# Kernel tuning notes

Measured on AMD Instinct MI355X. Metric: run time of the kernel, lower is better.

The kernel has to match this reference:

```python
import jax, jax.numpy as jnp
import numpy as np

NUM_HEADS = 8
LN_EPS = 1e-5


def setup_inputs() -> dict:
    key = jax.random.key(0)
    ks = jax.random.split(key, 8)
    B, H, W, C = 2, 64, 64, 256
    return {
        "x": jax.random.normal(ks[0], (B, H, W, C), dtype=jnp.float32),
        "cond": jax.random.normal(ks[1], (B, C), dtype=jnp.float32),
        "t": jax.random.randint(ks[2], (B,), 0, 100, dtype=jnp.int64),
        "emb_table": jax.random.normal(ks[3], (100, C), dtype=jnp.float32) * 0.02,
        "ada_w": jax.random.normal(ks[4], (C, 2 * C), dtype=jnp.float32) * 0.02,
        "ada_b": jnp.zeros((2 * C,), dtype=jnp.float32),
        "qkv_w": jax.random.normal(ks[5], (C, 3 * C), dtype=jnp.float32) * 0.02,
        "qkv_b": jnp.zeros((3 * C,), dtype=jnp.float32),
        "proj_w": jax.random.normal(ks[6], (C, C), dtype=jnp.float32) * 0.02,
        "proj_b": jnp.zeros((C,), dtype=jnp.float32),
    }


def reference(x, cond, t, emb_table, ada_w, ada_b, qkv_w, qkv_b, proj_w, proj_b):
    B, H, W, C = x.shape
    N = H * W
    h = NUM_HEADS
    d = C // h
    scale = d ** -0.5

    x = x.reshape(B, N, C)

    # AdaLayerNorm (adalayernorm_abs): timestep embedding -> SiLU -> Linear -> scale/shift
    emb = emb_table[t]                                # [B, C]
    ss = jax.nn.silu(emb) @ ada_w + ada_b             # [B, 2C]
    sc, sh = jnp.split(ss, 2, axis=-1)                # each [B, C]
    mu = jnp.mean(x, axis=-1, keepdims=True)
    var = jnp.var(x, axis=-1, keepdims=True)
    xn = (x - mu) * jax.lax.rsqrt(var + LN_EPS)       # LN without affine
    x = xn * (1.0 + sc[:, None, :]) + sh[:, None, :]

    # QKV projection and head split
    qkv = (x @ qkv_w + qkv_b).reshape(B, N, 3, h, d)
    qkv = jnp.transpose(qkv, (2, 0, 3, 1, 4))          # [3, B, h, N, d]
    q, k, v = qkv[0], qkv[1], qkv[2]

    # Manual attention: full [B, h, N, N] scores (matches original module)
    attn = jnp.einsum('bhnd,bhmd->bhnm', q, k) * scale
    attn = jax.nn.softmax(attn, axis=-1)
    out = jnp.einsum('bhnm,bhmd->bhnd', attn, v)       # [B, h, N, d]
    out = jnp.transpose(out, (0, 2, 1, 3)).reshape(B, N, C)

    out = (out.reshape(B, H, W, C) @ proj_w) + proj_b
    return out
```

## Files before the change

kernel.cpp:

```cpp
#include <hip/hip_runtime.h>
#include <hip/hip_bf16.h>
#include <stdint.h>

typedef __attribute__((ext_vector_type(8))) short bfrag;
typedef __attribute__((ext_vector_type(4))) short bfrag4;
typedef __attribute__((ext_vector_type(4))) float f32x4;
typedef __attribute__((ext_vector_type(2))) float f32x2;
typedef __attribute__((ext_vector_type(2))) unsigned int u32x2;

__device__ inline short f2bf(float f) {
  union { float f; uint32_t u; } v; v.f = f;
  uint32_t u = v.u;
  uint32_t r = (u + 0x7fffu + ((u >> 16) & 1u)) >> 16;
  return (short)r;
}

#if __has_builtin(__builtin_amdgcn_cvt_pk_bf16_f32)
typedef __attribute__((ext_vector_type(2))) __bf16 bf16x2_t;
__device__ inline uint32_t pack_bf16(float a, float b) {
  bf16x2_t r = __builtin_amdgcn_cvt_pk_bf16_f32(a, b);
  return __builtin_bit_cast(uint32_t, r);
}
#else
__device__ inline uint32_t pack_bf16(float a, float b) {
  uint32_t ua = __builtin_bit_cast(uint32_t, a) + 0x8000u;
  uint32_t ub = __builtin_bit_cast(uint32_t, b) + 0x8000u;
  return __builtin_amdgcn_perm(ub, ua, 0x07060302);
}
#endif

__global__ __launch_bounds__(256) void ada_kernel(
    const float* __restrict__ emb_table, const int* __restrict__ t,
    const float* __restrict__ ada_w, const float* __restrict__ ada_b,
    float* __restrict__ scsh) {
  int b = blockIdx.y;
  int tid = threadIdx.x;
  __shared__ float se[256];
  __shared__ float part[256];
  int tt = t[b];
  float e = emb_table[tt * 256 + tid];
  se[tid] = e / (1.f + __expf(-e));
  __syncthreads();
  int ol = tid & 63, kc = tid >> 6;
  int o = blockIdx.x * 64 + ol;
  float acc = 0.f;
#pragma unroll 8
  for (int k = kc * 64; k < (kc + 1) * 64; ++k) acc += se[k] * ada_w[k * 512 + o];
  part[tid] = acc;
  __syncthreads();
  if (tid < 64) {
    int oo = blockIdx.x * 64 + tid;
    scsh[b * 512 + oo] =
        part[tid] + part[64 + tid] + part[128 + tid] + part[192 + tid] + ada_b[oo];
  }
}

__global__ __launch_bounds__(256) void transpose_w(const float* __restrict__ W,
                                                   short* __restrict__ Wt, int N) {
  __shared__ float tile[64][65];
  int k0 = blockIdx.x * 64, n0 = blockIdx.y * 64;
  int tid = threadIdx.x;
  int r = tid >> 2, c0 = (tid & 3) * 16;
  const float* src = W + (long)(k0 + r) * N + n0 + c0;
#pragma unroll
  for (int j = 0; j < 16; j += 4) {
    float4 v = *(const float4*)(src + j);
    tile[r][c0 + j] = v.x; tile[r][c0 + j + 1] = v.y;
    tile[r][c0 + j + 2] = v.z; tile[r][c0 + j + 3] = v.w;
  }
  __syncthreads();
  int nl = tid >> 2, kc = (tid & 3) * 16;
  short outv[16];
#pragma unroll
  for (int j = 0; j < 16; ++j) outv[j] = f2bf(tile[kc + j][nl]);
  short* dst = Wt + (long)(n0 + nl) * 256 + k0 + kc;
  *(bfrag*)dst = *(bfrag*)&outv[0];
  *(bfrag*)(dst + 8) = *(bfrag*)&outv[8];
}

__global__ __launch_bounds__(256) void ln_kernel(const float* __restrict__ x,
                                                 const float* __restrict__ scsh,
                                                 short* __restrict__ xb) {
  int row = blockIdx.x;
  int b = row >> 12;
  int i = threadIdx.x;
  float v = x[(long)row * 256 + i];
  float s = v, sq = v * v;
#pragma unroll
  for (int off = 32; off > 0; off >>= 1) {
    s += __shfl_down(s, off);
    sq += __shfl_down(sq, off);
  }
  __shared__ float red[8];
  int w = i >> 6;
  if ((i & 63) == 0) { red[w] = s; red[4 + w] = sq; }
  __syncthreads();
  s = red[0] + red[1] + red[2] + red[3];
  sq = red[4] + red[5] + red[6] + red[7];
  float mu = s * (1.f / 256.f);
  float var = sq * (1.f / 256.f) - mu * mu;
  float xn = (v - mu) * rsqrtf(var + 1e-5f);
  float y = xn * (1.f + scsh[b * 512 + i]) + scsh[b * 512 + 256 + i];
  xb[(long)row * 256 + i] = f2bf(y);
}

__global__ __launch_bounds__(256) void gemm_bf16(const short* __restrict__ A,
                                                 const short* __restrict__ Bt,
                                                 const float* __restrict__ bias,
                                                 int N, int mode, float qscale,
                                                 short* __restrict__ qk,
                                                 short* __restrict__ vT,
                                                 float* __restrict__ cout) {
  __shared__ short As[64 * 40];
  __shared__ short Bs[64 * 40];
  const int mt = blockIdx.x, nt = blockIdx.y;
  const int tid = threadIdx.x;
  const int w = tid >> 6, lane = tid & 63, l16 = lane & 15, quad = lane >> 4;
  const int si = tid >> 2, sk = (tid & 3) * 8;
  f32x4 acc[4] = {{0,0,0,0},{0,0,0,0},{0,0,0,0},{0,0,0,0}};
  const short* Arow = A + (long)(mt * 64 + si) * 256 + sk;
  const short* Brow = Bt + (long)(nt * 64 + si) * 256 + sk;
  for (int kk = 0; kk < 8; ++kk) {
    __syncthreads();
    *(bfrag*)&As[si * 40 + sk] = *(const bfrag*)(Arow + kk * 32);
    *(bfrag*)&Bs[si * 40 + sk] = *(const bfrag*)(Brow + kk * 32);
    __syncthreads();
    bfrag a = *(const bfrag*)&As[(w * 16 + l16) * 40 + quad * 8];
#pragma unroll
    for (int c = 0; c < 4; ++c) {
      bfrag bf = *(const bfrag*)&Bs[(c * 16 + l16) * 40 + quad * 8];
      acc[c] = __builtin_amdgcn_mfma_f32_16x16x32_bf16(a, bf, acc[c], 0, 0, 0);
    }
  }
  const int row0 = mt * 64 + w * 16 + quad * 4;
  if (mode == 1) {
#pragma unroll
    for (int c = 0; c < 4; ++c) {
      int col = nt * 64 + c * 16 + l16;
      float bv = bias[col];
#pragma unroll
      for (int r = 0; r < 4; ++r)
        cout[(long)(row0 + r) * N + col] = acc[c][r] + bv;
    }
  } else if (nt < 8) {
#pragma unroll
    for (int c = 0; c < 4; ++c) {
      int col = nt * 64 + c * 16 + l16;
      float bv = bias[col];
      float mult = (col < 256) ? qscale : 1.0f;
#pragma unroll
      for (int r = 0; r < 4; ++r)
        qk[(long)(row0 + r) * 512 + col] = f2bf((acc[c][r] + bv) * mult);
    }
  } else {
    const int bb = mt >> 6;
    const int keyl = row0 & 4095;
#pragma unroll
    for (int c = 0; c < 4; ++c) {
      int col = nt * 64 + c * 16 + l16;
      float bv = bias[col];
      int d = col - 512;
      u32x2 dd;
      dd.x = pack_bf16(acc[c][0] + bv, acc[c][1] + bv);
      dd.y = pack_bf16(acc[c][2] + bv, acc[c][3] + bv);
      *(u32x2*)&vT[((long)(bb * 8 + (d >> 5)) * 32 + (d & 31)) * 4096 + keyl] = dd;
    }
  }
}

__global__ __launch_bounds__(256) void attn_kernel(const short* __restrict__ qk,
                                                   const short* __restrict__ vT,
                                                   float* __restrict__ Opart,
                                                   float* __restrict__ lpart) {
  const int blk = blockIdx.x;
  const int qt = blk & 31;
  const int bh = (blk >> 5) & 15;
  const int ks = blk >> 9;
  const int b = bh >> 3, hh = bh & 7;
  const int tid = threadIdx.x;
  const int w = tid >> 6, lane = tid & 63, l16 = lane & 15, quad = lane >> 4;

  __shared__ short Ks[2][64 * 40];
  __shared__ short Vt[2][32 * 68];

  const long rowbase = (long)b * 4096;
  const int qrow0 = qt * 128 + w * 32 + l16;
  bfrag qf0 = *(const bfrag*)&qk[(rowbase + qrow0) * 512 + hh * 32 + quad * 8];
  bfrag qf1 = *(const bfrag*)&qk[(rowbase + qrow0 + 16) * 512 + hh * 32 + quad * 8];

  f32x4 o00 = {0,0,0,0}, o10 = {0,0,0,0};
  f32x4 o01 = {0,0,0,0}, o11 = {0,0,0,0};
  f32x2 l0 = {0.f, 0.f}, l1 = {0.f, 0.f};

  const int si = tid >> 2, sk = (tid & 3) * 8;
  const int vrow = tid >> 3, vcol = (tid & 7) * 8;
  const short* ksrc = qk + rowbase * 512 + 256 + hh * 32 + (long)si * 512 + sk;
  const short* vsrc = vT + ((long)bh * 32 + vrow) * 4096 + vcol;

  const int kt0 = ks * 32;
  bfrag k8 = *(const bfrag*)(ksrc + (long)kt0 * 64 * 512);
  bfrag v8 = *(const bfrag*)(vsrc + kt0 * 64);

  int buf = 0;
  for (int i = 0; i < 32; ++i) {
    *(bfrag*)&Ks[buf][si * 40 + sk] = k8;
    *(bfrag*)&Vt[buf][vrow * 68 + vcol] = v8;
    int nn = (i < 31) ? (i + 1) : 31;
    k8 = *(const bfrag*)(ksrc + (long)(kt0 + nn) * 64 * 512);
    v8 = *(const bfrag*)(vsrc + (kt0 + nn) * 64);
    __syncthreads();

    f32x4 s0[4], s1[4];
#pragma unroll
    for (int nt = 0; nt < 4; ++nt) {
      bfrag kf = *(const bfrag*)&Ks[buf][(nt * 16 + l16) * 40 + quad * 8];
      f32x4 z = {0,0,0,0};
      s0[nt] = __builtin_amdgcn_mfma_f32_16x16x32_bf16(kf, qf0, z, 0, 0, 0);
      s1[nt] = __builtin_amdgcn_mfma_f32_16x16x32_bf16(kf, qf1, z, 0, 0, 0);
    }
    bfrag4 pb0[4], pb1[4];
#pragma unroll
    for (int nt = 0; nt < 4; ++nt) {
      float a0 = __builtin_amdgcn_exp2f(s0[nt][0]);
      float a1 = __builtin_amdgcn_exp2f(s0[nt][1]);
      float a2 = __builtin_amdgcn_exp2f(s0[nt][2]);
      float a3 = __builtin_amdgcn_exp2f(s0[nt][3]);
      f32x2 pa = {a0, a1}, pc = {a2, a3};
      l0 += pa; l0 += pc;
      u32x2 pk0; pk0.x = pack_bf16(a0, a1); pk0.y = pack_bf16(a2, a3);
      pb0[nt] = __builtin_bit_cast(bfrag4, pk0);
      float b0 = __builtin_amdgcn_exp2f(s1[nt][0]);
      float b1 = __builtin_amdgcn_exp2f(s1[nt][1]);
      float b2 = __builtin_amdgcn_exp2f(s1[nt][2]);
      float b3 = __builtin_amdgcn_exp2f(s1[nt][3]);
      f32x2 pb = {b0, b1}, pd = {b2, b3};
      l1 += pb; l1 += pd;
      u32x2 pk1; pk1.x = pack_bf16(b0, b1); pk1.y = pack_bf16(b2, b3);
      pb1[nt] = __builtin_bit_cast(bfrag4, pk1);
    }
#pragma unroll
    for (int nt = 0; nt < 4; ++nt) {
      bfrag4 va = *(const bfrag4*)&Vt[buf][l16 * 68 + nt * 16 + quad * 4];
      bfrag4 vb = *(const bfrag4*)&Vt[buf][(16 + l16) * 68 + nt * 16 + quad * 4];
      o00 = __builtin_amdgcn_mfma_f32_16x16x16bf16_1k(va, pb0[nt], o00, 0, 0, 0);
      o10 = __builtin_amdgcn_mfma_f32_16x16x16bf16_1k(vb, pb0[nt], o10, 0, 0, 0);
      o01 = __builtin_amdgcn_mfma_f32_16x16x16bf16_1k(va, pb1[nt], o01, 0, 0, 0);
      o11 = __builtin_amdgcn_mfma_f32_16x16x16bf16_1k(vb, pb1[nt], o11, 0, 0, 0);
    }
    buf ^= 1;
  }
  float ls0 = l0.x + l0.y, ls1 = l1.x + l1.y;
  ls0 += __shfl_xor(ls0, 16); ls0 += __shfl_xor(ls0, 32);
  ls1 += __shfl_xor(ls1, 16); ls1 += __shfl_xor(ls1, 32);
  const long pbase0 = (((long)ks * 16 + bh) * 4096 + qrow0) * 32;
  const long pbase1 = pbase0 + 16 * 32;
  *(f32x4*)&Opart[pbase0 + quad * 4] = o00;
  *(f32x4*)&Opart[pbase0 + 16 + quad * 4] = o10;
  *(f32x4*)&Opart[pbase1 + quad * 4] = o01;
  *(f32x4*)&Opart[pbase1 + 16 + quad * 4] = o11;
  if (quad == 0) {
    lpart[((long)ks * 16 + bh) * 4096 + qrow0] = ls0;
    lpart[((long)ks * 16 + bh) * 4096 + qrow0 + 16] = ls1;
  }
}

__global__ __launch_bounds__(256) void reduce_kernel(const float* __restrict__ Opart,
                                                     const float* __restrict__ lpart,
                                                     short* __restrict__ attn_out) {
  int row = blockIdx.x;
  int bq = row >> 12, q = row & 4095;
  int d = threadIdx.x;
  int h2 = d >> 5, dd = d & 31;
  int bh = bq * 8 + h2;
  long i0 = (((long)bh) * 4096 + q) * 32 + dd;
  long i1 = i0 + (long)16 * 4096 * 32;
  float l0 = lpart[(long)bh * 4096 + q];
  float l1 = lpart[(long)(16 + bh) * 4096 + q];
  float val = (Opart[i0] + Opart[i1]) / (l0 + l1);
  attn_out[(long)row * 256 + d] = f2bf(val);
}

extern "C" void kernel_launch(void* const* d_in, const int* in_sizes, int n_in,
                              void* d_out, int out_size, void* d_ws, size_t ws_size,
                              hipStream_t stream) {
  const float* x      = (const float*)d_in[0];
  const int*   t      = (const int*)d_in[2];
  const float* emb    = (const float*)d_in[3];
  const float* ada_w  = (const float*)d_in[4];
  const float* ada_b  = (const float*)d_in[5];
  const float* qkv_w  = (const float*)d_in[6];
  const float* qkv_b  = (const float*)d_in[7];
  const float* proj_w = (const float*)d_in[8];
  const float* proj_b = (const float*)d_in[9];

  char* ws = (char*)d_ws;
  float* scsh     = (float*)(ws);
  short* qkv_wt   = (short*)(ws + 4096);
  short* proj_wt  = (short*)(ws + 397312);
  short* xb       = (short*)(ws + 528384);
  short* qk_out   = (short*)(ws + 4722688);
  short* vT       = (short*)(ws + 13111296);
  short* attn_out = (short*)(ws + 17305600);
  float* Opart    = (float*)(ws + 21499904);
  float* lpart    = (float*)(ws + 38277120);

  const float QS = 0.17677669529663687f * 1.4426950408889634f;

  ada_kernel<<<dim3(8, 2), 256, 0, stream>>>(emb, t, ada_w, ada_b, scsh);
  transpose_w<<<dim3(4, 12), 256, 0, stream>>>(qkv_w, qkv_wt, 768);
  transpose_w<<<dim3(4, 4), 256, 0, stream>>>(proj_w, proj_wt, 256);
  ln_kernel<<<8192, 256, 0, stream>>>(x, scsh, xb);
  gemm_bf16<<<dim3(128, 12), 256, 0, stream>>>(xb, qkv_wt, qkv_b, 768, 0, QS,
                                               qk_out, vT, nullptr);
  attn_kernel<<<1024, 256, 0, stream>>>(qk_out, vT, Opart, lpart);
  reduce_kernel<<<8192, 256, 0, stream>>>(Opart, lpart, attn_out);
  gemm_bf16<<<dim3(128, 4), 256, 0, stream>>>(attn_out, proj_wt, proj_b, 256, 1,
                                              1.0f, nullptr, nullptr, (float*)d_out);
}
```

Measured before the change: 182.9 us.

## Merge prep kernels, enlarge GEMM M tile, split attention keys four ways with bf16 partials

```diff
diff --git a/kernel.cpp b/kernel.cpp
--- a/kernel.cpp
+++ b/kernel.cpp
@@ -14,6 +14,9 @@
   uint32_t r = (u + 0x7fffu + ((u >> 16) & 1u)) >> 16;
   return (short)r;
 }
+__device__ inline float bf2f(short s) {
+  return __builtin_bit_cast(float, (uint32_t)((uint32_t)(uint16_t)s << 16));
+}
 
 #if __has_builtin(__builtin_amdgcn_cvt_pk_bf16_f32)
 typedef __attribute__((ext_vector_type(2))) __bf16 bf16x2_t;
@@ -29,53 +32,58 @@
 }
 #endif
 
-__global__ __launch_bounds__(256) void ada_kernel(
+__global__ __launch_bounds__(256) void prep_kernel(
     const float* __restrict__ emb_table, const int* __restrict__ t,
     const float* __restrict__ ada_w, const float* __restrict__ ada_b,
-    float* __restrict__ scsh) {
-  int b = blockIdx.y;
-  int tid = threadIdx.x;
-  __shared__ float se[256];
-  __shared__ float part[256];
-  int tt = t[b];
-  float e = emb_table[tt * 256 + tid];
-  se[tid] = e / (1.f + __expf(-e));
-  __syncthreads();
-  int ol = tid & 63, kc = tid >> 6;
-  int o = blockIdx.x * 64 + ol;
-  float acc = 0.f;
+    float* __restrict__ scsh,
+    const float* __restrict__ qkv_w, short* __restrict__ qkv_wt,
+    const float* __restrict__ proj_w, short* __restrict__ proj_wt) {
+  __shared__ float smem[64 * 65];
+  const int blk = blockIdx.x;
+  const int tid = threadIdx.x;
+  if (blk < 16) {
+    float* se = smem;
+    float* part = smem + 256;
+    int b = blk >> 3, ox = blk & 7;
+    int tt = t[b];
+    float e = emb_table[tt * 256 + tid];
+    se[tid] = e / (1.f + __expf(-e));
+    __syncthreads();
+    int ol = tid & 63, kc = tid >> 6;
+    int o = ox * 64 + ol;
+    float acc = 0.f;
 #pragma unroll 8
-  for (int k = kc * 64; k < (kc + 1) * 64; ++k) acc += se[k] * ada_w[k * 512 + o];
-  part[tid] = acc;
-  __syncthreads();
-  if (tid < 64) {
-    int oo = blockIdx.x * 64 + tid;
-    scsh[b * 512 + oo] =
-        part[tid] + part[64 + tid] + part[128 + tid] + part[192 + tid] + ada_b[oo];
-  }
-}
-
-__global__ __launch_bounds__(256) void transpose_w(const float* __restrict__ W,
-                                                   short* __restrict__ Wt, int N) {
-  __shared__ float tile[64][65];
-  int k0 = blockIdx.x * 64, n0 = blockIdx.y * 64;
-  int tid = threadIdx.x;
-  int r = tid >> 2, c0 = (tid & 3) * 16;
-  const float* src = W + (long)(k0 + r) * N + n0 + c0;
-#pragma unroll
-  for (int j = 0; j < 16; j += 4) {
-    float4 v = *(const float4*)(src + j);
-    tile[r][c0 + j] = v.x; tile[r][c0 + j + 1] = v.y;
-    tile[r][c0 + j + 2] = v.z; tile[r][c0 + j + 3] = v.w;
-  }
-  __syncthreads();
-  int nl = tid >> 2, kc = (tid & 3) * 16;
-  short outv[16];
-#pragma unroll
-  for (int j = 0; j < 16; ++j) outv[j] = f2bf(tile[kc + j][nl]);
-  short* dst = Wt + (long)(n0 + nl) * 256 + k0 + kc;
-  *(bfrag*)dst = *(bfrag*)&outv[0];
-  *(bfrag*)(dst + 8) = *(bfrag*)&outv[8];
+    for (int k = kc * 64; k < (kc + 1) * 64; ++k) acc += se[k] * ada_w[k * 512 + o];
+    part[tid] = acc;
+    __syncthreads();
+    if (tid < 64) {
+      int oo = ox * 64 + tid;
+      scsh[b * 512 + oo] =
+          part[tid] + part[64 + tid] + part[128 + tid] + part[192 + tid] + ada_b[oo];
+    }
+  } else {
+    const float* W; short* Wt; int N, lb;
+    if (blk < 64) { W = qkv_w; Wt = qkv_wt; N = 768; lb = blk - 16; }
+    else          { W = proj_w; Wt = proj_wt; N = 256; lb = blk - 64; }
+    float (*tile)[65] = (float(*)[65])smem;
+    int k0 = (lb & 3) * 64, n0 = (lb >> 2) * 64;
+    int r = tid >> 2, c0 = (tid & 3) * 16;
+    const float* src = W + (long)(k0 + r) * N + n0 + c0;
+#pragma unroll
+    for (int j = 0; j < 16; j += 4) {
+      float4 v = *(const float4*)(src + j);
+      tile[r][c0 + j] = v.x; tile[r][c0 + j + 1] = v.y;
+      tile[r][c0 + j + 2] = v.z; tile[r][c0 + j + 3] = v.w;
+    }
+    __syncthreads();
+    int nl = tid >> 2, kc = (tid & 3) * 16;
+    short outv[16];
+#pragma unroll
+    for (int j = 0; j < 16; ++j) outv[j] = f2bf(tile[kc + j][nl]);
+    short* dst = Wt + (long)(n0 + nl) * 256 + k0 + kc;
+    *(bfrag*)dst = *(bfrag*)&outv[0];
+    *(bfrag*)(dst + 8) = *(bfrag*)&outv[8];
+  }
 }
 
 __global__ __launch_bounds__(256) void ln_kernel(const float* __restrict__ x,
@@ -111,67 +119,82 @@
                                                  short* __restrict__ qk,
                                                  short* __restrict__ vT,
                                                  float* __restrict__ cout) {
-  __shared__ short As[64 * 40];
+  __shared__ short As[128 * 40];
   __shared__ short Bs[64 * 40];
   const int mt = blockIdx.x, nt = blockIdx.y;
   const int tid = threadIdx.x;
   const int w = tid >> 6, lane = tid & 63, l16 = lane & 15, quad = lane >> 4;
-  const int si = tid >> 2, sk = (tid & 3) * 8;
-  f32x4 acc[4] = {{0,0,0,0},{0,0,0,0},{0,0,0,0},{0,0,0,0}};
-  const short* Arow = A + (long)(mt * 64 + si) * 256 + sk;
-  const short* Brow = Bt + (long)(nt * 64 + si) * 256 + sk;
+  const int ar = tid >> 1, ak = (tid & 1) * 16;
+  const int br = tid >> 2, bk = (tid & 3) * 8;
+  f32x4 acc[2][4] = {};
+  const short* Arow = A + (long)(mt * 128 + ar) * 256 + ak;
+  const short* Brow = Bt + (long)(nt * 64 + br) * 256 + bk;
   for (int kk = 0; kk < 8; ++kk) {
     __syncthreads();
-    *(bfrag*)&As[si * 40 + sk] = *(const bfrag*)(Arow + kk * 32);
-    *(bfrag*)&Bs[si * 40 + sk] = *(const bfrag*)(Brow + kk * 32);
-    __syncthreads();
-    bfrag a = *(const bfrag*)&As[(w * 16 + l16) * 40 + quad * 8];
+    *(bfrag*)&As[ar * 40 + ak] = *(const bfrag*)(Arow + kk * 32);
+    *(bfrag*)&As[ar * 40 + ak + 8] = *(const bfrag*)(Arow + kk * 32 + 8);
+    *(bfrag*)&Bs[br * 40 + bk] = *(const bfrag*)(Brow + kk * 32);
+    __syncthreads();
+    bfrag a0 = *(const bfrag*)&As[(w * 32 + l16) * 40 + quad * 8];
+    bfrag a1 = *(const bfrag*)&As[(w * 32 + 16 + l16) * 40 + quad * 8];
 #pragma unroll
     for (int c = 0; c < 4; ++c) {
       bfrag bf = *(const bfrag*)&Bs[(c * 16 + l16) * 40 + quad * 8];
-      acc[c] = __builtin_amdgcn_mfma_f32_16x16x32_bf16(a, bf, acc[c], 0, 0, 0);
-    }
-  }
-  const int row0 = mt * 64 + w * 16 + quad * 4;
+      acc[0][c] = __builtin_amdgcn_mfma_f32_16x16x32_bf16(a0, bf, acc[0][c], 0, 0, 0);
+      acc[1][c] = __builtin_amdgcn_mfma_f32_16x16x32_bf16(a1, bf, acc[1][c], 0, 0, 0);
+    }
+  }
+  const int rowb = mt * 128 + w * 32 + quad * 4;
   if (mode == 1) {
 #pragma unroll
-    for (int c = 0; c < 4; ++c) {
-      int col = nt * 64 + c * 16 + l16;
-      float bv = bias[col];
-#pragma unroll
-      for (int r = 0; r < 4; ++r)
-        cout[(long)(row0 + r) * N + col] = acc[c][r] + bv;
+    for (int rg = 0; rg < 2; ++rg) {
+      int row0 = rowb + rg * 16;
+#pragma unroll
+      for (int c = 0; c < 4; ++c) {
+        int col = nt * 64 + c * 16 + l16;
+        float bv = bias[col];
+#pragma unroll
+        for (int r = 0; r < 4; ++r)
+          cout[(long)(row0 + r) * N + col] = acc[rg][c][r] + bv;
+      }
     }
   } else if (nt < 8) {
 #pragma unroll
-    for (int c = 0; c < 4; ++c) {
-      int col = nt * 64 + c * 16 + l16;
-      float bv = bias[col];
-      float mult = (col < 256) ? qscale : 1.0f;
-#pragma unroll
-      for (int r = 0; r < 4; ++r)
-        qk[(long)(row0 + r) * 512 + col] = f2bf((acc[c][r] + bv) * mult);
+    for (int rg = 0; rg < 2; ++rg) {
+      int row0 = rowb + rg * 16;
+#pragma unroll
+      for (int c = 0; c < 4; ++c) {
+        int col = nt * 64 + c * 16 + l16;
+        float bv = bias[col];
+        float mult = (col < 256) ? qscale : 1.0f;
+#pragma unroll
+        for (int r = 0; r < 4; ++r)
+          qk[(long)(row0 + r) * 512 + col] = f2bf((acc[rg][c][r] + bv) * mult);
+      }
     }
   } else {
-    const int bb = mt >> 6;
-    const int keyl = row0 & 4095;
-#pragma unroll
-    for (int c = 0; c < 4; ++c) {
-      int col = nt * 64 + c * 16 + l16;
-      float bv = bias[col];
-      int d = col - 512;
-      u32x2 dd;
-      dd.x = pack_bf16(acc[c][0] + bv, acc[c][1] + bv);
-      dd.y = pack_bf16(acc[c][2] + bv, acc[c][3] + bv);
-      *(u32x2*)&vT[((long)(bb * 8 + (d >> 5)) * 32 + (d & 31)) * 4096 + keyl] = dd;
-    }
-  }
-}
-
-__global__ __launch_bounds__(256) void attn_kernel(const short* __restrict__ qk,
-                                                   const short* __restrict__ vT,
-                                                   float* __restrict__ Opart,
-                                                   float* __restrict__ lpart) {
+    const int bb = mt >> 5;
+#pragma unroll
+    for (int rg = 0; rg < 2; ++rg) {
+      int keyl = (rowb + rg * 16) & 4095;
+#pragma unroll
+      for (int c = 0; c < 4; ++c) {
+        int col = nt * 64 + c * 16 + l16;
+        float bv = bias[col];
+        int d = col - 512;
+        u32x2 dd;
+        dd.x = pack_bf16(acc[rg][c][0] + bv, acc[rg][c][1] + bv);
+        dd.y = pack_bf16(acc[rg][c][2] + bv, acc[rg][c][3] + bv);
+        *(u32x2*)&vT[((long)(bb * 8 + (d >> 5)) * 32 + (d & 31)) * 4096 + keyl] = dd;
+      }
+    }
+  }
+}
+
+__global__ __launch_bounds__(256, 8) void attn_kernel(const short* __restrict__ qk,
+                                                      const short* __restrict__ vT,
+                                                      short* __restrict__ OpB,
+                                                      float* __restrict__ lpart) {
   const int blk = blockIdx.x;
   const int qt = blk & 31;
   const int bh = (blk >> 5) & 15;
@@ -197,15 +220,15 @@
   const short* ksrc = qk + rowbase * 512 + 256 + hh * 32 + (long)si * 512 + sk;
   const short* vsrc = vT + ((long)bh * 32 + vrow) * 4096 + vcol;
 
-  const int kt0 = ks * 32;
+  const int kt0 = ks * 16;
   bfrag k8 = *(const bfrag*)(ksrc + (long)kt0 * 64 * 512);
   bfrag v8 = *(const bfrag*)(vsrc + kt0 * 64);
 
   int buf = 0;
-  for (int i = 0; i < 32; ++i) {
+  for (int i = 0; i < 16; ++i) {
     *(bfrag*)&Ks[buf][si * 40 + sk] = k8;
     *(bfrag*)&Vt[buf][vrow * 68 + vcol] = v8;
-    int nn = (i < 31) ? (i + 1) : 31;
+    int nn = (i < 15) ? (i + 1) : 15;
     k8 = *(const bfrag*)(ksrc + (long)(kt0 + nn) * 64 * 512);
     v8 = *(const bfrag*)(vsrc + (kt0 + nn) * 64);
     __syncthreads();
@@ -252,19 +275,24 @@
   float ls0 = l0.x + l0.y, ls1 = l1.x + l1.y;
   ls0 += __shfl_xor(ls0, 16); ls0 += __shfl_xor(ls0, 32);
   ls1 += __shfl_xor(ls1, 16); ls1 += __shfl_xor(ls1, 32);
-  const long pbase0 = (((long)ks * 16 + bh) * 4096 + qrow0) * 32;
-  const long pbase1 = pbase0 + 16 * 32;
-  *(f32x4*)&Opart[pbase0 + quad * 4] = o00;
-  *(f32x4*)&Opart[pbase0 + 16 + quad * 4] = o10;
-  *(f32x4*)&Opart[pbase1 + quad * 4] = o01;
-  *(f32x4*)&Opart[pbase1 + 16 + quad * 4] = o11;
+  const long pb0 = (((long)ks * 16 + bh) * 4096 + qrow0) * 32;
+  const long pb1 = pb0 + 16 * 32;
+  u32x2 dA, dB, dC, dD;
+  dA.x = pack_bf16(o00[0], o00[1]); dA.y = pack_bf16(o00[2], o00[3]);
+  dB.x = pack_bf16(o10[0], o10[1]); dB.y = pack_bf16(o10[2], o10[3]);
+  dC.x = pack_bf16(o01[0], o01[1]); dC.y = pack_bf16(o01[2], o01[3]);
+  dD.x = pack_bf16(o11[0], o11[1]); dD.y = pack_bf16(o11[2], o11[3]);
+  *(u32x2*)&OpB[pb0 + quad * 4] = dA;
+  *(u32x2*)&OpB[pb0 + 16 + quad * 4] = dB;
+  *(u32x2*)&OpB[pb1 + quad * 4] = dC;
+  *(u32x2*)&OpB[pb1 + 16 + quad * 4] = dD;
   if (quad == 0) {
     lpart[((long)ks * 16 + bh) * 4096 + qrow0] = ls0;
     lpart[((long)ks * 16 + bh) * 4096 + qrow0 + 16] = ls1;
   }
 }
 
-__global__ __launch_bounds__(256) void reduce_kernel(const float* __restrict__ Opart,
+__global__ __launch_bounds__(256) void reduce_kernel(const short* __restrict__ OpB,
                                                      const float* __restrict__ lpart,
                                                      short* __restrict__ attn_out) {
   int row = blockIdx.x;
@@ -272,12 +300,14 @@
   int d = threadIdx.x;
   int h2 = d >> 5, dd = d & 31;
   int bh = bq * 8 + h2;
-  long i0 = (((long)bh) * 4096 + q) * 32 + dd;
-  long i1 = i0 + (long)16 * 4096 * 32;
-  float l0 = lpart[(long)bh * 4096 + q];
-  float l1 = lpart[(long)(16 + bh) * 4096 + q];
-  float val = (Opart[i0] + Opart[i1]) / (l0 + l1);
-  attn_out[(long)row * 256 + d] = f2bf(val);
+  float s = 0.f, l = 0.f;
+#pragma unroll
+  for (int ks = 0; ks < 4; ++ks) {
+    long base = (long)(ks * 16 + bh) * 4096 + q;
+    s += bf2f(OpB[base * 32 + dd]);
+    l += lpart[base];
+  }
+  attn_out[(long)row * 256 + d] = f2bf(s / l);
 }
 
 extern "C" void kernel_launch(void* const* d_in, const int* in_sizes, int n_in,
@@ -301,19 +331,18 @@
   short* qk_out   = (short*)(ws + 4722688);
   short* vT       = (short*)(ws + 13111296);
   short* attn_out = (short*)(ws + 17305600);
-  float* Opart    = (float*)(ws + 21499904);
+  short* OpB      = (short*)(ws + 21499904);
   float* lpart    = (float*)(ws + 38277120);
 
   const float QS = 0.17677669529663687f * 1.4426950408889634f;
 
-  ada_kernel<<<dim3(8, 2), 256, 0, stream>>>(emb, t, ada_w, ada_b, scsh);
-  transpose_w<<<dim3(4, 12), 256, 0, stream>>>(qkv_w, qkv_wt, 768);
-  transpose_w<<<dim3(4, 4), 256, 0, stream>>>(proj_w, proj_wt, 256);
+  prep_kernel<<<80, 256, 0, stream>>>(emb, t, ada_w, ada_b, scsh,
+                                      qkv_w, qkv_wt, proj_w, proj_wt);
   ln_kernel<<<8192, 256, 0, stream>>>(x, scsh, xb);
-  gemm_bf16<<<dim3(128, 12), 256, 0, stream>>>(xb, qkv_wt, qkv_b, 768, 0, QS,
-                                               qk_out, vT, nullptr);
-  attn_kernel<<<1024, 256, 0, stream>>>(qk_out, vT, Opart, lpart);
-  reduce_kernel<<<8192, 256, 0, stream>>>(Opart, lpart, attn_out);
-  gemm_bf16<<<dim3(128, 4), 256, 0, stream>>>(attn_out, proj_wt, proj_b, 256, 1,
-                                              1.0f, nullptr, nullptr, (float*)d_out);
-}
+  gemm_bf16<<<dim3(64, 12), 256, 0, stream>>>(xb, qkv_wt, qkv_b, 768, 0, QS,
+                                              qk_out, vT, nullptr);
+  attn_kernel<<<2048, 256, 0, stream>>>(qk_out, vT, OpB, lpart);
+  reduce_kernel<<<8192, 256, 0, stream>>>(OpB, lpart, attn_out);
+  gemm_bf16<<<dim3(64, 4), 256, 0, stream>>>(attn_out, proj_wt, proj_b, 256, 1,
+                                             1.0f, nullptr, nullptr, (float*)d_out);
+}
```

Measured after the change: 260.8 us. 42.6% more time.
